# Kernel tuning notes

Measured on AMD Instinct MI355X. Metric: run time of the kernel, lower is better.

Reference implementation:

```python
import jax, jax.numpy as jnp
import numpy as np

NUM_HEADS = 32
NUM_KV_HEADS = 8
HEAD_DIM = 128
ROPE_THETA = 10000.0


def _rope_cos_sin(seq_len, head_dim, dtype):
    # [seq, head_dim/2] angles, duplicated to [seq, head_dim] via concat (rotate-half convention)
    inv_freq = 1.0 / (ROPE_THETA ** (jnp.arange(0, head_dim, 2, dtype=jnp.float32) / head_dim))
    ang = jnp.arange(seq_len, dtype=jnp.float32)[:, None] * inv_freq[None, :]
    ang = jnp.concatenate([ang, ang], axis=-1)
    return jnp.cos(ang).astype(dtype), jnp.sin(ang).astype(dtype)


def _rotate_half(x):
    d = x.shape[-1] // 2
    return jnp.concatenate([-x[..., d:], x[..., :d]], axis=-1)


def setup_inputs() -> dict:
    key = jax.random.key(0)
    ks = jax.random.split(key, 5)
    E = NUM_HEADS * HEAD_DIM
    KVE = NUM_KV_HEADS * HEAD_DIM
    B, S = 2, 2048
    sc_in = 1.0 / np.sqrt(E)
    return {
        "x": jax.random.normal(ks[0], (B, S, E), jnp.float32),
        "Wq": jax.random.normal(ks[1], (E, E), jnp.float32) * sc_in,
        "Wk": jax.random.normal(ks[2], (E, KVE), jnp.float32) * sc_in,
        "Wv": jax.random.normal(ks[3], (E, KVE), jnp.float32) * sc_in,
        "Wo": jax.random.normal(ks[4], (E, E), jnp.float32) * sc_in,
    }


def reference(x, Wq, Wk, Wv, Wo):
    b, s, e = x.shape
    H, KV, D = NUM_HEADS, NUM_KV_HEADS, HEAD_DIM
    G = H // KV
    scale = 1.0 / np.sqrt(D)

    q = (x @ Wq).reshape(b, s, H, D).transpose(0, 2, 1, 3)    # [b,H,s,D]
    k = (x @ Wk).reshape(b, s, KV, D).transpose(0, 2, 1, 3)   # [b,KV,s,D]
    v = (x @ Wv).reshape(b, s, KV, D).transpose(0, 2, 1, 3)   # [b,KV,s,D]

    cos, sin = _rope_cos_sin(s, D, q.dtype)                   # [s,D]
    q = q * cos + _rotate_half(q) * sin
    k = k * cos + _rotate_half(k) * sin

    # GQA: group q heads by kv head instead of repeat_interleaving k/v
    qg = q.reshape(b, KV, G, s, D)
    attn = jnp.einsum("bkgqd,bkvd->bkgqv", qg, k) * scale     # [b,KV,G,s,s]

    causal = jnp.where(
        jnp.arange(s)[:, None] >= jnp.arange(s)[None, :], 0.0, -jnp.inf
    ).astype(jnp.float32)
    attn = attn.astype(jnp.float32) + causal
    attn = jax.nn.softmax(attn, axis=-1).astype(q.dtype)

    out = jnp.einsum("bkgqv,bkvd->bkgqd", attn, v)            # [b,KV,G,s,D]
    out = out.reshape(b, H, s, D).transpose(0, 2, 1, 3).reshape(b, s, H * D)
    return out @ Wo
```

## Files before the change

kernel.cpp:

```cpp
#include <hip/hip_runtime.h>
#include <stdint.h>
#include <math.h>

typedef short bf16x8 __attribute__((ext_vector_type(8)));
typedef float f32x4 __attribute__((ext_vector_type(4)));

#if __has_builtin(__builtin_amdgcn_exp2f)
#define EXP2F(x) __builtin_amdgcn_exp2f(x)
#else
#define EXP2F(x) exp2f(x)
#endif

static constexpr int Bn   = 2;
static constexpr int Sn   = 2048;
static constexpr int NH   = 32;
static constexpr int NKV  = 8;
static constexpr int Dh   = 128;
static constexpr int En   = NH * Dh;
static constexpr int KVEn = NKV * Dh;
static constexpr int QKVE = En + 2 * KVEn;
static constexpr int MT   = Bn * Sn;
static constexpr int QT   = Sn / 128;

__device__ __forceinline__ unsigned short f2bf(float f) {
  unsigned int u = __float_as_uint(f);
  u += 0x7FFFu + ((u >> 16) & 1u);
  return (unsigned short)(u >> 16);
}
__device__ __forceinline__ float bf2f(unsigned short h) {
  return __uint_as_float(((unsigned int)h) << 16);
}

typedef __attribute__((address_space(1))) void* gas_t;
typedef __attribute__((address_space(3))) void* las_t;
__device__ __forceinline__ void gl_lds16(const void* g, void* l) {
  __builtin_amdgcn_global_load_lds((gas_t)(uintptr_t)g, (las_t)(uint32_t)(uintptr_t)l,
                                   16, 0, 0);
}

#define VMW(n)  asm volatile("s_waitcnt vmcnt(" #n ")" ::: "memory")
#define LGKM0   asm volatile("s_waitcnt lgkmcnt(0)" ::: "memory")
#define SCHEDB  __builtin_amdgcn_sched_barrier(0)
#define BAR     __builtin_amdgcn_s_barrier()


__global__ void cast_bf16_kernel(const float* __restrict__ x,
                                 unsigned short* __restrict__ y, int n4) {
  int i = blockIdx.x * 256 + threadIdx.x;
  if (i >= n4) return;
  float4 v = ((const float4*)x)[i];
  ushort4 o;
  o.x = f2bf(v.x); o.y = f2bf(v.y); o.z = f2bf(v.z); o.w = f2bf(v.w);
  ((ushort4*)y)[i] = o;
}

__global__ void tcast_kernel(const float* __restrict__ W,
                             unsigned short* __restrict__ WT, int R, int C) {
  __shared__ float t[32][33];
  int tx = threadIdx.x, ty = threadIdx.y;
  int c = blockIdx.x * 32 + tx, r = blockIdx.y * 32 + ty;
  t[ty][tx] = W[(size_t)r * C + c];
  __syncthreads();
  int ro = blockIdx.x * 32 + ty, co = blockIdx.y * 32 + tx;
  WT[(size_t)ro * R + co] = f2bf(t[tx][ty]);
}

__global__ void rope_table_kernel(float2* __restrict__ cs) {
  int i = blockIdx.x * 256 + threadIdx.x;
  int s = i >> 6, d = i & 63;
  float inv = powf(10000.0f, -(float)d * (1.0f / 64.0f));
  float a = (float)s * inv;
  cs[i] = make_float2(cosf(a), sinf(a));
}

__global__ void rope_kernel(unsigned short* __restrict__ q,
                            const float2* __restrict__ cs, int rowstride, float scl) {
  int row = blockIdx.x;
  int s = row & (Sn - 1);
  int hl = threadIdx.x >> 6, d = threadIdx.x & 63;
  int h = blockIdx.y * 4 + hl;
  size_t base = (size_t)row * rowstride + (size_t)h * Dh + d;
  float2 c = cs[s * 64 + d];
  float x0 = bf2f(q[base]), x1 = bf2f(q[base + 64]);
  q[base]      = f2bf((x0 * c.x - x1 * c.y) * scl);
  q[base + 64] = f2bf((x1 * c.x + x0 * c.y) * scl);
}

__global__ void vtrans_kernel(const unsigned short* __restrict__ V, int rowstride,
                              unsigned short* __restrict__ Vt) {
  __shared__ unsigned short t[32][33];
  int bk = blockIdx.z;
  int b = bk >> 3, kv = bk & 7;
  int d = blockIdx.x * 32 + threadIdx.x;
  int s = blockIdx.y * 32 + threadIdx.y;
  t[threadIdx.y][threadIdx.x] = V[(size_t)(b * Sn + s) * rowstride + kv * Dh + d];
  __syncthreads();
  int dd = blockIdx.x * 32 + threadIdx.y;
  int so = blockIdx.y * 32 + threadIdx.x;
  Vt[((size_t)bk * Dh + dd) * Sn + so] = t[threadIdx.x][threadIdx.y];
}


__global__ __launch_bounds__(512, 2) void gemm256_kernel(
    const unsigned short* __restrict__ A, const unsigned short* __restrict__ BT,
    void* __restrict__ Cout, int M, int N, int K, int out_f32) {
  __shared__ unsigned short lds[2][4][128 * 64];
  const int tid = threadIdx.x;
  const int lane = tid & 63, wave = tid >> 6;
  const int r15 = lane & 15, kg = lane >> 4;
  const int wr = wave >> 2, wc = wave & 3;
  const int m0 = blockIdx.y * 256, n0 = blockIdx.x * 256;
  const char* Ab = (const char*)A;
  const char* Bb = (const char*)BT;
  const int KT = K >> 6;

  f32x4 acc[2][2][4][2] = {};
  bf16x8 ar[4][2];
  bf16x8 br[2][2][2];

#define STAGE_H(SRC, ROW0, KT_, SLOT)                                         \
  do {                                                                        \
    _Pragma("unroll") for (int ld = 0; ld < 2; ++ld) {                        \
      int _f = (ld * 512 + tid) * 16;                                         \
      int _row = _f >> 7, _cb = _f & 127;                                     \
      gl_lds16(SRC + ((size_t)((ROW0) + _row) * K + (size_t)(KT_) * 64) * 2 + \
                   (_cb ^ ((_row & 7) << 4)),                                 \
               (char*)(SLOT) + _f);                                           \
    }                                                                         \
  } while (0)

#define GPHASE(MH, NH, BUF, DO_LDA, DO_LDB, STAGE_STMT, WAIT_STMT)            \
  do {                                                                        \
    if (DO_LDA) {                                                             \
      const char* _as = (const char*)lds[BUF][MH];                            \
      _Pragma("unroll") for (int mf = 0; mf < 4; ++mf) {                      \
        int _r = wr * 64 + mf * 16 + r15;                                     \
        int _sw = (_r & 7) << 4;                                              \
        ar[mf][0] = *(const bf16x8*)(_as + _r * 128 + ((kg * 16) ^ _sw));     \
        ar[mf][1] = *(const bf16x8*)(_as + _r * 128 + ((64 + kg * 16) ^ _sw));\
      }                                                                       \
    }                                                                         \
    if (DO_LDB) {                                                             \
      const char* _bs = (const char*)lds[BUF][2 + NH];                        \
      _Pragma("unroll") for (int nf = 0; nf < 2; ++nf) {                      \
        int _r = wc * 32 + nf * 16 + r15;                                     \
        int _sw = (_r & 7) << 4;                                              \
        br[NH][nf][0] =                                                       \
            *(const bf16x8*)(_bs + _r * 128 + ((kg * 16) ^ _sw));             \
        br[NH][nf][1] =                                                       \
            *(const bf16x8*)(_bs + _r * 128 + ((64 + kg * 16) ^ _sw));        \
      }                                                                       \
    }                                                                         \
    STAGE_STMT;                                                               \
    BAR;                                                                      \
    if ((DO_LDA) || (DO_LDB)) { LGKM0; }                                      \
    SCHEDB;                                                                   \
    __builtin_amdgcn_s_setprio(1);                                            \
    _Pragma("unroll") for (int mf = 0; mf < 4; ++mf)                          \
      _Pragma("unroll") for (int n2 = 0; n2 < 2; ++n2) {                      \
        acc[MH][NH][mf][n2] = __builtin_amdgcn_mfma_f32_16x16x32_bf16(        \
            ar[mf][0], br[NH][n2][0], acc[MH][NH][mf][n2], 0, 0, 0);          \
        acc[MH][NH][mf][n2] = __builtin_amdgcn_mfma_f32_16x16x32_bf16(        \
            ar[mf][1], br[NH][n2][1], acc[MH][NH][mf][n2], 0, 0, 0);          \
      }                                                                       \
    __builtin_amdgcn_s_setprio(0);                                            \
    SCHEDB;                                                                   \
    WAIT_STMT;                                                                \
    BAR;                                                                      \
    SCHEDB;                                                                   \
  } while (0)

  STAGE_H(Ab, m0,       0, lds[0][0]);
  STAGE_H(Bb, n0,       0, lds[0][2]);
  STAGE_H(Ab, m0 + 128, 0, lds[0][1]);
  STAGE_H(Bb, n0 + 128, 0, lds[0][3]);
  STAGE_H(Ab, m0,       1, lds[1][0]);
  STAGE_H(Bb, n0,       1, lds[1][2]);
  VMW(8);
  SCHEDB;
  BAR;
  SCHEDB;

  for (int k = 0; k + 2 < KT; k += 2) {
    GPHASE(0, 0, 0, true,  true,  STAGE_H(Ab, m0 + 128, k + 1, lds[1][1]), VMW(6));
    GPHASE(0, 1, 0, false, true,  STAGE_H(Bb, n0 + 128, k + 1, lds[1][3]), VMW(10));
    GPHASE(1, 0, 0, true,  false, STAGE_H(Ab, m0,       k + 2, lds[0][0]), (void)0);
    GPHASE(1, 1, 0, false, false, STAGE_H(Bb, n0,       k + 2, lds[0][2]), VMW(8));
    GPHASE(0, 0, 1, true,  true,  STAGE_H(Ab, m0 + 128, k + 2, lds[0][1]), VMW(6));
    GPHASE(0, 1, 1, false, true,  STAGE_H(Bb, n0 + 128, k + 2, lds[0][3]), VMW(10));
    GPHASE(1, 0, 1, true,  false, STAGE_H(Ab, m0,       k + 3, lds[1][0]), (void)0);
    GPHASE(1, 1, 1, false, false, STAGE_H(Bb, n0,       k + 3, lds[1][2]), VMW(8));
  }
  GPHASE(0, 0, 0, true,  true,  STAGE_H(Ab, m0 + 128, KT - 1, lds[1][1]), VMW(6));
  GPHASE(0, 1, 0, false, true,  STAGE_H(Bb, n0 + 128, KT - 1, lds[1][3]), VMW(10));
  GPHASE(1, 0, 0, true,  false, (void)0, (void)0);
  GPHASE(1, 1, 0, false, false, (void)0, VMW(0));
  GPHASE(0, 0, 1, true,  true,  (void)0, (void)0);
  GPHASE(0, 1, 1, false, true,  (void)0, (void)0);
  GPHASE(1, 0, 1, true,  false, (void)0, (void)0);
  GPHASE(1, 1, 1, false, false, (void)0, (void)0);

#undef GPHASE
#undef STAGE_H

#pragma unroll
  for (int mh = 0; mh < 2; ++mh)
#pragma unroll
    for (int nh = 0; nh < 2; ++nh)
#pragma unroll
      for (int mf = 0; mf < 4; ++mf)
#pragma unroll
        for (int nf = 0; nf < 2; ++nf)
#pragma unroll
          for (int t = 0; t < 4; ++t) {
            int row = m0 + mh * 128 + wr * 64 + mf * 16 + kg * 4 + t;
            int col = n0 + nh * 128 + wc * 32 + nf * 16 + r15;
            if (out_f32)
              ((float*)Cout)[(size_t)row * N + col] = acc[mh][nh][mf][nf][t];
            else
              ((unsigned short*)Cout)[(size_t)row * N + col] =
                  f2bf(acc[mh][nh][mf][nf][t]);
          }
}


__device__ __forceinline__ void sm_update(f32x4 sc[4], f32x4 o[8],
                                          float mrow[4], float lrow[4],
                                          bool diag, int qrow0, int kt,
                                          int r15, int kg, char* Pw) {
  if (diag) {
#pragma unroll
    for (int kf = 0; kf < 4; ++kf) {
      int kvg = kt * 64 + kf * 16 + r15;
#pragma unroll
      for (int t = 0; t < 4; ++t)
        if (kvg > qrow0 + kg * 4 + t) sc[kf][t] = -1e30f;
    }
  }
  float mx[4], sm[4];
#pragma unroll
  for (int t = 0; t < 4; ++t) {
    float v = fmaxf(fmaxf(sc[0][t], sc[1][t]), fmaxf(sc[2][t], sc[3][t]));
#pragma unroll
    for (int off = 1; off < 16; off <<= 1) v = fmaxf(v, __shfl_xor(v, off, 16));
    mx[t] = fmaxf(mrow[t], v);
    sm[t] = EXP2F(mrow[t] - mx[t]);
    mrow[t] = mx[t];
  }
#pragma unroll
  for (int kf = 0; kf < 4; ++kf)
#pragma unroll
    for (int t = 0; t < 4; ++t) sc[kf][t] = EXP2F(sc[kf][t] - mx[t]);
#pragma unroll
  for (int t = 0; t < 4; ++t) {
    float v = sc[0][t] + sc[1][t] + sc[2][t] + sc[3][t];
#pragma unroll
    for (int off = 1; off < 16; off <<= 1) v += __shfl_xor(v, off, 16);
    lrow[t] = lrow[t] * sm[t] + v;
  }
#pragma unroll
  for (int nf = 0; nf < 8; ++nf)
#pragma unroll
    for (int t = 0; t < 4; ++t) o[nf][t] *= sm[t];
#pragma unroll
  for (int kf = 0; kf < 4; ++kf)
#pragma unroll
    for (int t = 0; t < 4; ++t) {
      int r = kg * 4 + t, c = kf * 16 + r15;
      *(unsigned short*)(Pw + r * 128 + ((c * 2) ^ ((r & 7) << 4))) = f2bf(sc[kf][t]);
    }
}

__global__ __launch_bounds__(512, 4) void attn_kernel(
    const unsigned short* __restrict__ Q, const unsigned short* __restrict__ Kl,
    const unsigned short* __restrict__ Vt, unsigned short* __restrict__ AO) {
  __shared__ unsigned short Ks[2][64 * 128];
  __shared__ unsigned short Vs[2][128 * 64];
  __shared__ unsigned short Ps[8][16 * 64];
  const int tid = threadIdx.x, lane = tid & 63, wave = tid >> 6;
  const int h = blockIdx.x, b = blockIdx.z;
  const int qt = (QT - 1) - blockIdx.y;
  const int kvh = h >> 2;
  const int r15 = lane & 15, kg = lane >> 4;
  const int qrow0 = qt * 128 + wave * 16;
  const int kmax = 2 * qt + 2;

  bf16x8 qf[4];
#pragma unroll
  for (int db = 0; db < 4; ++db)
    qf[db] = *(const bf16x8*)&Q[(size_t)(b * Sn + qrow0 + r15) * QKVE +
                                h * Dh + db * 32 + kg * 8];

  f32x4 o[8] = {};
  float mrow[4] = {-1e30f, -1e30f, -1e30f, -1e30f};
  float lrow[4] = {0.f, 0.f, 0.f, 0.f};

  const char* Kbase = (const char*)Kl + (size_t)(b * Sn) * (QKVE * 2) + kvh * 256;
  const char* Vbase = (const char*)Vt + (size_t)((b * NKV + kvh) * Dh) * (Sn * 2);

  auto stage = [&](int kt, int bi) {
#pragma unroll
    for (int c = 0; c < 2; ++c) {
      int f = (c * 512 + tid) * 16;
      int row = f >> 8, cb = f & 255;
      gl_lds16(Kbase + (size_t)(kt * 64 + row) * (QKVE * 2) + (cb ^ ((row & 7) << 4)),
               (char*)Ks[bi] + f);
    }
#pragma unroll
    for (int c = 0; c < 2; ++c) {
      int f = (c * 512 + tid) * 16;
      int row = f >> 7, cb = f & 127;
      gl_lds16(Vbase + (size_t)row * (Sn * 2) + kt * 128 + (cb ^ ((row & 7) << 4)),
               (char*)Vs[bi] + f);
    }
  };

  stage(0, 0);
  __syncthreads();

  for (int kt = 0; kt < kmax; ++kt) {
    const int cur = kt & 1;
    if (kt + 1 < kmax) stage(kt + 1, cur ^ 1);
    if (kt * 64 <= qrow0 + 15) {
      const char* Kc = (const char*)Ks[cur];
      const char* Vc = (const char*)Vs[cur];
      f32x4 sc[4] = {};
      __builtin_amdgcn_s_setprio(1);
#pragma unroll
      for (int db = 0; db < 4; ++db) {
#pragma unroll
        for (int kf = 0; kf < 4; ++kf) {
          int krow = kf * 16 + r15;
          int cb = (db * 32 + kg * 8) * 2;
          bf16x8 kb = *(const bf16x8*)(Kc + krow * 256 + (cb ^ ((krow & 7) << 4)));
          sc[kf] = __builtin_amdgcn_mfma_f32_16x16x32_bf16(qf[db], kb, sc[kf], 0, 0, 0);
        }
      }
      __builtin_amdgcn_s_setprio(0);

      char* Pw = (char*)Ps[wave];
      bool diag = (kt * 64 + 63) > qrow0;
      sm_update(sc, o, mrow, lrow, diag, qrow0, kt, r15, kg, Pw);

      __builtin_amdgcn_s_setprio(1);
#pragma unroll
      for (int ks = 0; ks < 2; ++ks) {
        bf16x8 pa = *(const bf16x8*)(Pw + r15 * 128 + ((kg * 16 + ks * 64) ^ ((r15 & 7) << 4)));
#pragma unroll
        for (int nf = 0; nf < 8; ++nf) {
          int vrow = nf * 16 + r15;
          int cb = (ks * 32 + kg * 8) * 2;
          bf16x8 vb = *(const bf16x8*)(Vc + vrow * 128 + (cb ^ ((vrow & 7) << 4)));
          o[nf] = __builtin_amdgcn_mfma_f32_16x16x32_bf16(pa, vb, o[nf], 0, 0, 0);
        }
      }
      __builtin_amdgcn_s_setprio(0);
    }
    __syncthreads();
  }

  float rinv[4];
#pragma unroll
  for (int t = 0; t < 4; ++t) rinv[t] = 1.0f / lrow[t];
#pragma unroll
  for (int nf = 0; nf < 8; ++nf)
#pragma unroll
    for (int t = 0; t < 4; ++t) {
      int srow = qrow0 + kg * 4 + t;
      AO[(size_t)(b * Sn + srow) * En + h * Dh + nf * 16 + r15] = f2bf(o[nf][t] * rinv[t]);
    }
}


extern "C" void kernel_launch(void* const* d_in, const int* in_sizes, int n_in,
                              void* d_out, int out_size, void* d_ws, size_t ws_size,
                              hipStream_t stream) {
  const float* x  = (const float*)d_in[0];
  const float* Wq = (const float*)d_in[1];
  const float* Wk = (const float*)d_in[2];
  const float* Wv = (const float*)d_in[3];
  const float* Wo = (const float*)d_in[4];

  char* ws = (char*)d_ws;
  size_t off = 0;
  auto alloc = [&](size_t bytes) -> char* {
    char* p = ws + off;
    off += (bytes + 255) & ~(size_t)255;
    return p;
  };
  unsigned short* xb   = (unsigned short*)alloc((size_t)MT * En * 2);
  unsigned short* Wqkv = (unsigned short*)alloc((size_t)QKVE * En * 2);
  unsigned short* WoT  = (unsigned short*)alloc((size_t)En * En * 2);
  unsigned short* Cqkv = (unsigned short*)alloc((size_t)MT * QKVE * 2);
  unsigned short* Vt   = (unsigned short*)alloc((size_t)MT * KVEn * 2);
  float2* cs           = (float2*)alloc((size_t)Sn * 64 * sizeof(float2));
  unsigned short* AO   = xb;

  cast_bf16_kernel<<<MT * (En / 4) / 256, 256, 0, stream>>>(x, xb, MT * En / 4);
  tcast_kernel<<<dim3(En / 32, En / 32), dim3(32, 32), 0, stream>>>(Wq, Wqkv, En, En);
  tcast_kernel<<<dim3(KVEn / 32, En / 32), dim3(32, 32), 0, stream>>>(
      Wk, Wqkv + (size_t)En * En, En, KVEn);
  tcast_kernel<<<dim3(KVEn / 32, En / 32), dim3(32, 32), 0, stream>>>(
      Wv, Wqkv + (size_t)(En + KVEn) * En, En, KVEn);
  tcast_kernel<<<dim3(En / 32, En / 32), dim3(32, 32), 0, stream>>>(Wo, WoT, En, En);
  rope_table_kernel<<<Sn * 64 / 256, 256, 0, stream>>>(cs);

  gemm256_kernel<<<dim3(QKVE / 256, MT / 256), 512, 0, stream>>>(
      xb, Wqkv, Cqkv, MT, QKVE, En, 0);

  const float scl = 0.08838834764831845f * 1.4426950408889634f;
  rope_kernel<<<dim3(MT, NH / 4), 256, 0, stream>>>(Cqkv, cs, QKVE, scl);
  rope_kernel<<<dim3(MT, NKV / 4), 256, 0, stream>>>(Cqkv + En, cs, QKVE, 1.0f);
  vtrans_kernel<<<dim3(Dh / 32, Sn / 32, Bn * NKV), dim3(32, 32), 0, stream>>>(
      Cqkv + En + KVEn, QKVE, Vt);

  attn_kernel<<<dim3(NH, QT, Bn), 512, 0, stream>>>(Cqkv, Cqkv + En, Vt, AO);

  gemm256_kernel<<<dim3(En / 256, MT / 256), 512, 0, stream>>>(
      AO, WoT, d_out, MT, En, En, 1);
}
```

Measured before the change: 615.8 us.

## Vectorize weight transpose-cast and RoPE, add lazy softmax rescaling in attention

```diff
diff --git a/kernel.cpp b/kernel.cpp
--- a/kernel.cpp
+++ b/kernel.cpp
@@ -56,13 +56,27 @@
 
 __global__ void tcast_kernel(const float* __restrict__ W,
                              unsigned short* __restrict__ WT, int R, int C) {
-  __shared__ float t[32][33];
-  int tx = threadIdx.x, ty = threadIdx.y;
-  int c = blockIdx.x * 32 + tx, r = blockIdx.y * 32 + ty;
-  t[ty][tx] = W[(size_t)r * C + c];
+  __shared__ float t[64][69];
+  int tx = threadIdx.x & 15, ty = threadIdx.x >> 4;
+  int r0 = blockIdx.y * 64, c0 = blockIdx.x * 64;
+#pragma unroll
+  for (int i = 0; i < 4; ++i) {
+    float4 v = *(const float4*)&W[(size_t)(r0 + ty * 4 + i) * C + (c0 + tx * 4)];
+    t[ty * 4 + i][tx * 4 + 0] = v.x;
+    t[ty * 4 + i][tx * 4 + 1] = v.y;
+    t[ty * 4 + i][tx * 4 + 2] = v.z;
+    t[ty * 4 + i][tx * 4 + 3] = v.w;
+  }
   __syncthreads();
-  int ro = blockIdx.x * 32 + ty, co = blockIdx.y * 32 + tx;
-  WT[(size_t)ro * R + co] = f2bf(t[tx][ty]);
+#pragma unroll
+  for (int i = 0; i < 4; ++i) {
+    ushort4 o;
+    o.x = f2bf(t[tx * 4 + 0][ty * 4 + i]);
+    o.y = f2bf(t[tx * 4 + 1][ty * 4 + i]);
+    o.z = f2bf(t[tx * 4 + 2][ty * 4 + i]);
+    o.w = f2bf(t[tx * 4 + 3][ty * 4 + i]);
+    *(ushort4*)&WT[(size_t)(c0 + ty * 4 + i) * R + (r0 + tx * 4)] = o;
+  }
 }
 
 __global__ void rope_table_kernel(float2* __restrict__ cs) {
@@ -77,13 +91,21 @@
                             const float2* __restrict__ cs, int rowstride, float scl) {
   int row = blockIdx.x;
   int s = row & (Sn - 1);
-  int hl = threadIdx.x >> 6, d = threadIdx.x & 63;
-  int h = blockIdx.y * 4 + hl;
-  size_t base = (size_t)row * rowstride + (size_t)h * Dh + d;
-  float2 c = cs[s * 64 + d];
-  float x0 = bf2f(q[base]), x1 = bf2f(q[base + 64]);
-  q[base]      = f2bf((x0 * c.x - x1 * c.y) * scl);
-  q[base + 64] = f2bf((x1 * c.x + x0 * c.y) * scl);
+  int h = threadIdx.x >> 3, d0 = (threadIdx.x & 7) * 8;
+  size_t base = (size_t)row * rowstride + (size_t)h * Dh + d0;
+  bf16x8 lo = *(const bf16x8*)&q[base];
+  bf16x8 hi = *(const bf16x8*)&q[base + 64];
+  bf16x8 olo, ohi;
+#pragma unroll
+  for (int e = 0; e < 8; ++e) {
+    float2 c = cs[s * 64 + d0 + e];
+    float x0 = bf2f((unsigned short)lo[e]);
+    float x1 = bf2f((unsigned short)hi[e]);
+    olo[e] = (short)f2bf((x0 * c.x - x1 * c.y) * scl);
+    ohi[e] = (short)f2bf((x1 * c.x + x0 * c.y) * scl);
+  }
+  *(bf16x8*)&q[base] = olo;
+  *(bf16x8*)&q[base + 64] = ohi;
 }
 
 __global__ void vtrans_kernel(const unsigned short* __restrict__ V, int rowstride,
@@ -237,31 +259,38 @@
         if (kvg > qrow0 + kg * 4 + t) sc[kf][t] = -1e30f;
     }
   }
-  float mx[4], sm[4];
+  float nm[4];
+  bool grow = false;
 #pragma unroll
   for (int t = 0; t < 4; ++t) {
     float v = fmaxf(fmaxf(sc[0][t], sc[1][t]), fmaxf(sc[2][t], sc[3][t]));
 #pragma unroll
     for (int off = 1; off < 16; off <<= 1) v = fmaxf(v, __shfl_xor(v, off, 16));
-    mx[t] = fmaxf(mrow[t], v);
-    sm[t] = EXP2F(mrow[t] - mx[t]);
-    mrow[t] = mx[t];
+    nm[t] = v;
+    grow = grow || (v > mrow[t] + 8.0f);
+  }
+  if (__any(grow)) {
+#pragma unroll
+    for (int t = 0; t < 4; ++t) {
+      float mx = fmaxf(mrow[t], nm[t]);
+      float sm = EXP2F(mrow[t] - mx);
+      mrow[t] = mx;
+      lrow[t] *= sm;
+#pragma unroll
+      for (int nf = 0; nf < 8; ++nf) o[nf][t] *= sm;
+    }
   }
 #pragma unroll
   for (int kf = 0; kf < 4; ++kf)
 #pragma unroll
-    for (int t = 0; t < 4; ++t) sc[kf][t] = EXP2F(sc[kf][t] - mx[t]);
+    for (int t = 0; t < 4; ++t) sc[kf][t] = EXP2F(sc[kf][t] - mrow[t]);
 #pragma unroll
   for (int t = 0; t < 4; ++t) {
     float v = sc[0][t] + sc[1][t] + sc[2][t] + sc[3][t];
 #pragma unroll
     for (int off = 1; off < 16; off <<= 1) v += __shfl_xor(v, off, 16);
-    lrow[t] = lrow[t] * sm[t] + v;
-  }
-#pragma unroll
-  for (int nf = 0; nf < 8; ++nf)
-#pragma unroll
-    for (int t = 0; t < 4; ++t) o[nf][t] *= sm[t];
+    lrow[t] += v;
+  }
 #pragma unroll
   for (int kf = 0; kf < 4; ++kf)
 #pragma unroll
@@ -397,20 +426,20 @@
   unsigned short* AO   = xb;
 
   cast_bf16_kernel<<<MT * (En / 4) / 256, 256, 0, stream>>>(x, xb, MT * En / 4);
-  tcast_kernel<<<dim3(En / 32, En / 32), dim3(32, 32), 0, stream>>>(Wq, Wqkv, En, En);
-  tcast_kernel<<<dim3(KVEn / 32, En / 32), dim3(32, 32), 0, stream>>>(
+  tcast_kernel<<<dim3(En / 64, En / 64), 256, 0, stream>>>(Wq, Wqkv, En, En);
+  tcast_kernel<<<dim3(KVEn / 64, En / 64), 256, 0, stream>>>(
       Wk, Wqkv + (size_t)En * En, En, KVEn);
-  tcast_kernel<<<dim3(KVEn / 32, En / 32), dim3(32, 32), 0, stream>>>(
+  tcast_kernel<<<dim3(KVEn / 64, En / 64), 256, 0, stream>>>(
       Wv, Wqkv + (size_t)(En + KVEn) * En, En, KVEn);
-  tcast_kernel<<<dim3(En / 32, En / 32), dim3(32, 32), 0, stream>>>(Wo, WoT, En, En);
+  tcast_kernel<<<dim3(En / 64, En / 64), 256, 0, stream>>>(Wo, WoT, En, En);
   rope_table_kernel<<<Sn * 64 / 256, 256, 0, stream>>>(cs);
 
   gemm256_kernel<<<dim3(QKVE / 256, MT / 256), 512, 0, stream>>>(
       xb, Wqkv, Cqkv, MT, QKVE, En, 0);
 
   const float scl = 0.08838834764831845f * 1.4426950408889634f;
-  rope_kernel<<<dim3(MT, NH / 4), 256, 0, stream>>>(Cqkv, cs, QKVE, scl);
-  rope_kernel<<<dim3(MT, NKV / 4), 256, 0, stream>>>(Cqkv + En, cs, QKVE, 1.0f);
+  rope_kernel<<<MT, 256, 0, stream>>>(Cqkv, cs, QKVE, scl);
+  rope_kernel<<<MT, 64, 0, stream>>>(Cqkv + En, cs, QKVE, 1.0f);
   vtrans_kernel<<<dim3(Dh / 32, Sn / 32, Bn * NKV), dim3(32, 32), 0, stream>>>(
       Cqkv + En + KVEn, QKVE, Vt);
 
```

Result: faster. 572.9 us (-7.0%).
